# Kernel tuning notes

Measured on AMD Instinct MI355X. Metric: run time of the kernel, lower is better.

## Reference

```python
import jax, jax.numpy as jnp
import numpy as np

H, E, N, R = 1024, 2048, 16, 64  # hidden, expand, state, dt_rank
B, L = 2, 2048


def setup_inputs() -> dict:
    key = jax.random.key(0)
    ks = jax.random.split(key, 20)
    s = 0.02
    inp = {
        "x": jax.random.normal(ks[0], (B, L, H), jnp.float32),
        "ln_gamma": jnp.ones((H,), jnp.float32),
        "ln_beta": jnp.zeros((H,), jnp.float32),
        "W_in": jax.random.normal(ks[1], (H, 2 * E), jnp.float32) * s,
        "b_in": jnp.zeros((2 * E,), jnp.float32),
        "W_delta": jax.random.normal(ks[2], (E, R), jnp.float32) * s,
        "b_delta": jnp.zeros((R,), jnp.float32),
        "W_dt": jax.random.normal(ks[3], (R, E), jnp.float32) * s,
        "b_dt": jnp.zeros((E,), jnp.float32),
        "W_B": jax.random.normal(ks[4], (E, N), jnp.float32) * s,
        "b_B": jnp.zeros((N,), jnp.float32),
        "W_C": jax.random.normal(ks[5], (E, N), jnp.float32) * s,
        "b_C": jnp.zeros((N,), jnp.float32),
        "A_log": -jnp.exp(jax.random.normal(ks[6], (E, N), jnp.float32) * 0.1),
        "D": jax.random.normal(ks[7], (E,), jnp.float32) * 0.1,
        "W_out": jax.random.normal(ks[8], (E, H), jnp.float32) * s,
        "b_out": jnp.zeros((H,), jnp.float32),
    }
    return inp


def _layer_norm(x, gamma, beta, eps=1e-5):
    mu = jnp.mean(x, axis=-1, keepdims=True)
    var = jnp.var(x, axis=-1, keepdims=True)
    return (x - mu) * jax.lax.rsqrt(var + eps) * gamma + beta


def _selective_scan(x, delta, A, Bm, Cm):
    # x, delta: [B,L,E]; Bm, Cm: [B,L,N]; A: [E,N]
    def step(h, inputs):
        x_t, d_t, B_t, C_t = inputs  # [B,E],[B,E],[B,N],[B,N]
        A_disc = jnp.exp(d_t[..., None] * A)                     # [B,E,N]
        h = A_disc * h + d_t[..., None] * B_t[:, None, :] * x_t[..., None]
        y_t = jnp.einsum('bn,ben->be', C_t, h)
        return h, y_t

    h0 = jnp.zeros((x.shape[0], A.shape[0], A.shape[1]), x.dtype)
    xs = (jnp.swapaxes(x, 0, 1), jnp.swapaxes(delta, 0, 1),
          jnp.swapaxes(Bm, 0, 1), jnp.swapaxes(Cm, 0, 1))
    _, ys = jax.lax.scan(step, h0, xs)  # ys: [L,B,E]
    return jnp.swapaxes(ys, 0, 1)


def reference(x, ln_gamma, ln_beta, W_in, b_in, W_delta, b_delta, W_dt, b_dt,
              W_B, b_B, W_C, b_C, A_log, D, W_out, b_out):
    residual = x
    xn = _layer_norm(x, ln_gamma, ln_beta)
    x_proj = xn @ W_in + b_in                     # [B,L,2E]
    u, gate = jnp.split(x_proj, 2, axis=-1)
    u = jax.nn.silu(u)
    delta = jax.nn.softplus((u @ W_delta + b_delta) @ W_dt + b_dt)  # [B,L,E]
    Bm = u @ W_B + b_B                            # [B,L,N]
    Cm = u @ W_C + b_C                            # [B,L,N]
    A = -jnp.exp(A_log)                           # [E,N]
    y = _selective_scan(u, delta, A, Bm, Cm)
    y = y + u * D
    y = y * jax.nn.silu(gate)
    return y @ W_out + b_out + residual
```

## Files before the change

### kernel.cpp

```cpp
#include <hip/hip_runtime.h>
#include <stdint.h>

#define DH 1024
#define DE 2048
#define DN 16
#define DR 64
#define DB 2
#define DL 2048
#define DT (DB * DL)

typedef short short8 __attribute__((ext_vector_type(8)));
typedef float f32x4 __attribute__((ext_vector_type(4)));

__device__ __forceinline__ float bf2f(uint32_t u) {
  union { uint32_t i; float f; } v; v.i = u << 16; return v.f;
}
__device__ __forceinline__ unsigned short f2bf(float f) {
  union { float f; uint32_t i; } v; v.f = f;
  uint32_t r = v.i + 0x7FFFu + ((v.i >> 16) & 1u);
  return (unsigned short)(r >> 16);
}
__device__ __forceinline__ float ldsc(const void* p, size_t i, bool f32) {
  return f32 ? ((const float*)p)[i] : bf2f(((const unsigned short*)p)[i]);
}
__device__ __forceinline__ float4 ld4(const void* p, size_t i, bool f32) {
  if (f32) return *(const float4*)((const float*)p + i);
  ushort4 v = *(const ushort4*)((const unsigned short*)p + i);
  return make_float4(bf2f(v.x), bf2f(v.y), bf2f(v.z), bf2f(v.w));
}

__device__ __forceinline__ void gll16(const unsigned short* g, unsigned short* l) {
  __builtin_amdgcn_global_load_lds(
      (const __attribute__((address_space(1))) unsigned int*)g,
      (__attribute__((address_space(3))) unsigned int*)l, 16, 0, 0);
}

__device__ __forceinline__ void transpose_tile(
    const void* src, unsigned short* dst, int K, int N, int bx, int by,
    int tid, bool f32, float (*tile)[33]) {
  const int tx = tid & 31;
  const int ty = tid >> 5;
  const int kb = by * 32, nb = bx * 32;
  #pragma unroll
  for (int i = 0; i < 4; ++i)
    tile[ty + 8 * i][tx] = ldsc(src, (size_t)(kb + ty + 8 * i) * N + nb + tx, f32);
  __syncthreads();
  #pragma unroll
  for (int i = 0; i < 4; ++i)
    dst[(size_t)(nb + ty + 8 * i) * K + kb + tx] = f2bf(tile[tx][ty + 8 * i]);
}

__global__ __launch_bounds__(256) void k_convert_all(
    const void* __restrict__ W_in, const void* __restrict__ W_out,
    const void* __restrict__ W_dt, const void* __restrict__ Wd,
    const void* __restrict__ Wb, const void* __restrict__ Wc,
    const void* __restrict__ b_in, const void* __restrict__ b_out,
    const void* __restrict__ b_delta, const void* __restrict__ b_B,
    const void* __restrict__ b_C, const void* __restrict__ A_log,
    const void* __restrict__ Dvec, const void* __restrict__ b_dt,
    unsigned short* __restrict__ WtIn, unsigned short* __restrict__ WtOut,
    unsigned short* __restrict__ WtDt, unsigned short* __restrict__ WtDbc,
    float* __restrict__ bin, float* __restrict__ bout,
    float* __restrict__ bdbc, float* __restrict__ Ac, float* __restrict__ Dv,
    float* __restrict__ bdt,
    const uint32_t* __restrict__ probe) {
  const bool f32 = (probe[0] == 0x3F800000u);
  __shared__ float tile[32][33];
  const int tid = threadIdx.x;
  int f = blockIdx.x;
  if (f < 4096) {
    transpose_tile(W_in, WtIn, 1024, 4096, f & 127, f >> 7, tid, f32, tile);
    return;
  }
  f -= 4096;
  if (f < 2048) {
    transpose_tile(W_out, WtOut, 2048, 1024, f & 31, f >> 5, tid, f32, tile);
    return;
  }
  f -= 2048;
  if (f < 128) {
    transpose_tile(W_dt, WtDt, 64, 2048, f & 63, f >> 6, tid, f32, tile);
    return;
  }
  f -= 128;
  if (f < 1024) {
    const int idx = f * 256 + tid;
    const int c = idx >> 11, k = idx & 2047;
    float v = 0.f;
    if (c < 64) v = ldsc(Wd, (size_t)k * DR + c, f32);
    else if (c < 80) v = ldsc(Wb, (size_t)k * DN + (c - 64), f32);
    else if (c < 96) v = ldsc(Wc, (size_t)k * DN + (c - 80), f32);
    WtDbc[idx] = f2bf(v);
    return;
  }
  f -= 1024;
  {
    int i = f * 256 + tid;
    if (i < 4096) { bin[i] = ldsc(b_in, i, f32); return; }
    i -= 4096;
    if (i < 1024) { bout[i] = ldsc(b_out, i, f32); return; }
    i -= 1024;
    if (i < 128) {
      float v = 0.f;
      if (i < 64) v = ldsc(b_delta, i, f32);
      else if (i < 80) v = ldsc(b_B, i - 64, f32);
      else if (i < 96) v = ldsc(b_C, i - 80, f32);
      bdbc[i] = v; return;
    }
    i -= 128;
    if (i < 32768) { Ac[i] = -__expf(ldsc(A_log, i, f32)); return; }
    i -= 32768;
    if (i < 2048) { Dv[i] = ldsc(Dvec, i, f32); return; }
    i -= 2048;
    if (i < 2048) { bdt[i] = ldsc(b_dt, i, f32); }
  }
}

__global__ __launch_bounds__(256) void k_dbc_reduce(
    const float* __restrict__ Part, const float* __restrict__ bdbc,
    unsigned short* __restrict__ dt1b, float* __restrict__ dtBC, int MT) {
  const int gid = blockIdx.x * 256 + threadIdx.x;
  const int row = gid / 96, col = gid - row * 96;
  if (row >= MT) return;
  float s = bdbc[col];
  const size_t stride = (size_t)MT * 96;
  #pragma unroll
  for (int kp = 0; kp < 8; ++kp)
    s += Part[(size_t)kp * stride + (size_t)row * 96 + col];
  if (col < 64) dt1b[(size_t)row * 64 + col] = f2bf(s);
  else dtBC[(size_t)row * 32 + (col - 64)] = s;
}

__global__ __launch_bounds__(256) void k_delta(
    const unsigned short* __restrict__ A,
    const unsigned short* __restrict__ Wt,
    const float* __restrict__ bdt,
    unsigned short* __restrict__ Dout) {
  const int tid = threadIdx.x;
  const int wid = tid >> 6;
  const int lane = tid & 63;
  const int quad = lane >> 4;
  const int l16 = lane & 15;
  const int r0 = blockIdx.y * 32 + (wid & 1) * 16;
  const int c0 = blockIdx.x * 128 + (wid >> 1) * 64;

  const unsigned short* ap = A + (size_t)(r0 + l16) * 64 + quad * 8;
  const short8 a0 = *(const short8*)(ap);
  const short8 a1 = *(const short8*)(ap + 32);

  f32x4 acc[4];
  #pragma unroll
  for (int j = 0; j < 4; ++j) {
    acc[j][0] = 0.f; acc[j][1] = 0.f; acc[j][2] = 0.f; acc[j][3] = 0.f;
  }
  #pragma unroll
  for (int j = 0; j < 4; ++j) {
    const unsigned short* bp = Wt + (size_t)(c0 + j * 16 + l16) * 64 + quad * 8;
    const short8 b0 = *(const short8*)(bp);
    const short8 b1 = *(const short8*)(bp + 32);
    acc[j] = __builtin_amdgcn_mfma_f32_16x16x32_bf16(a0, b0, acc[j], 0, 0, 0);
    acc[j] = __builtin_amdgcn_mfma_f32_16x16x32_bf16(a1, b1, acc[j], 0, 0, 0);
  }
  #pragma unroll
  for (int j = 0; j < 4; ++j) {
    const int col = c0 + j * 16 + l16;
    const float bs = bdt[col];
    #pragma unroll
    for (int r = 0; r < 4; ++r) {
      const int row = r0 + quad * 4 + r;
      const float v = acc[j][r] + bs;
      const float sp = fmaxf(v, 0.f) + __logf(1.f + __expf(-fabsf(v)));
      Dout[(size_t)row * 2048 + col] = f2bf(sp);
    }
  }
}

__global__ __launch_bounds__(256) void k_out_reduce(
    const float* __restrict__ Part2, const float* __restrict__ bout,
    const void* __restrict__ resid, void* __restrict__ dout,
    int MT, int t0, int lgTc, const uint32_t* __restrict__ probe) {
  const bool f32 = (probe[0] == 0x3F800000u);
  const int gid = blockIdx.x * 256 + threadIdx.x;
  const int base = gid * 4;
  const int row = base >> 10;
  const int col = base & 1023;
  if (row >= MT) return;
  const int tcm = (1 << lgTc) - 1;
  const size_t grow = (size_t)((row >> lgTc) * DL + t0 + (row & tcm));
  const size_t ms = (size_t)MT * 1024;
  float4 p0 = *(const float4*)(Part2 + (size_t)row * 1024 + col);
  float4 p1 = *(const float4*)(Part2 + ms + (size_t)row * 1024 + col);
  float4 bo = *(const float4*)(bout + col);
  float4 rs = ld4(resid, grow * 1024 + col, f32);
  float4 o;
  o.x = p0.x + p1.x + bo.x + rs.x;
  o.y = p0.y + p1.y + bo.y + rs.y;
  o.z = p0.z + p1.z + bo.z + rs.z;
  o.w = p0.w + p1.w + bo.w + rs.w;
  if (f32) {
    *(float4*)((float*)dout + grow * 1024 + col) = o;
  } else {
    ushort4 u;
    u.x = f2bf(o.x); u.y = f2bf(o.y); u.z = f2bf(o.z); u.w = f2bf(o.w);
    *(ushort4*)((unsigned short*)dout + grow * 1024 + col) = u;
  }
}

__global__ __launch_bounds__(256) void ln_bf16(
    const void* __restrict__ x, const void* __restrict__ gamma,
    const void* __restrict__ beta, unsigned short* __restrict__ xn,
    int t0, int lgTc, const uint32_t* __restrict__ probe) {
  const bool f32 = (probe[0] == 0x3F800000u);
  const int row = blockIdx.x;
  const int tid = threadIdx.x;
  const int tcm = (1 << lgTc) - 1;
  const int grow = (row >> lgTc) * DL + t0 + (row & tcm);
  float4 v = ld4(x, (size_t)grow * DH + tid * 4, f32);
  float s = v.x + v.y + v.z + v.w;
  float ss = v.x * v.x + v.y * v.y + v.z * v.z + v.w * v.w;
  #pragma unroll
  for (int off = 32; off > 0; off >>= 1) {
    s += __shfl_down(s, off, 64);
    ss += __shfl_down(ss, off, 64);
  }
  __shared__ float sbuf[4], ssbuf[4];
  const int wave = tid >> 6, lane = tid & 63;
  if (lane == 0) { sbuf[wave] = s; ssbuf[wave] = ss; }
  __syncthreads();
  float tot = sbuf[0] + sbuf[1] + sbuf[2] + sbuf[3];
  float tots = ssbuf[0] + ssbuf[1] + ssbuf[2] + ssbuf[3];
  const float inv = 1.0f / (float)DH;
  float mu = tot * inv;
  float var = tots * inv - mu * mu;
  float rs = rsqrtf(var + 1e-5f);
  float4 gv = ld4(gamma, tid * 4, f32);
  float4 bv = ld4(beta, tid * 4, f32);
  ushort4 o;
  o.x = f2bf((v.x - mu) * rs * gv.x + bv.x);
  o.y = f2bf((v.y - mu) * rs * gv.y + bv.y);
  o.z = f2bf((v.z - mu) * rs * gv.z + bv.z);
  o.w = f2bf((v.w - mu) * rs * gv.w + bv.w);
  *(ushort4*)(xn + (size_t)row * DH + tid * 4) = o;
}

__global__ __launch_bounds__(256) void gemm_mfma(
    const unsigned short* __restrict__ A, int lda,
    const unsigned short* __restrict__ Wt,
    const float* __restrict__ bias,
    const void* __restrict__ resid,
    void* __restrict__ C, int ldc,
    int K, int mode, int t0, int lgTc,
    const uint32_t* __restrict__ probe) {
  __shared__ unsigned short As[2][4096];
  __shared__ unsigned short Bs[2][4096];
  const int tid = threadIdx.x;
  const int wid = tid >> 6;
  const int lane = tid & 63;
  const int quad = lane >> 4;
  const int l16 = lane & 15;
  const int wm = (wid & 1) * 64;
  const int wn = (wid >> 1) * 64;
  const int m0 = blockIdx.y * 128;
  int n0 = blockIdx.x * 128;
  int kbeg = 0, kend = K;
  if (mode == 5) {
    const int Ks = K >> 3; kbeg = blockIdx.x * Ks; kend = kbeg + Ks; n0 = 0;
  } else if (mode == 6) {
    const int Ks = K >> 1; const int kp = blockIdx.x >> 3;
    kbeg = kp * Ks; kend = kbeg + Ks; n0 = (blockIdx.x & 7) * 128;
  }
  const int sr = tid >> 2;
  const int sc = (tid & 3) * 8;

  const unsigned short* gA0 = A + (size_t)(m0 + sr) * lda + sc;
  const unsigned short* gA1 = A + (size_t)(m0 + sr + 64) * lda + sc;
  const unsigned short* gB0 = Wt + (size_t)(n0 + sr) * K + sc;
  const unsigned short* gB1 = Wt + (size_t)(n0 + sr + 64) * K + sc;
  const int wb = (tid & 192) * 8;
  unsigned short* lA00 = &As[0][wb];
  unsigned short* lA01 = &As[1][wb];
  unsigned short* lA10 = &As[0][2048 + wb];
  unsigned short* lA11 = &As[1][2048 + wb];
  unsigned short* lB00 = &Bs[0][wb];
  unsigned short* lB01 = &Bs[1][wb];
  unsigned short* lB10 = &Bs[0][2048 + wb];
  unsigned short* lB11 = &Bs[1][2048 + wb];

  f32x4 acc[4][4];
  #pragma unroll
  for (int i = 0; i < 4; ++i)
    #pragma unroll
    for (int j = 0; j < 4; ++j) {
      acc[i][j][0] = 0.f; acc[i][j][1] = 0.f;
      acc[i][j][2] = 0.f; acc[i][j][3] = 0.f;
    }

  for (int k0 = kbeg; k0 < kend; k0 += 64) {
    gll16(gA0 + k0, lA00);
    gll16(gA0 + k0 + 32, lA01);
    gll16(gA1 + k0, lA10);
    gll16(gA1 + k0 + 32, lA11);
    gll16(gB0 + k0, lB00);
    gll16(gB0 + k0 + 32, lB01);
    gll16(gB1 + k0, lB10);
    gll16(gB1 + k0 + 32, lB11);
    __syncthreads();
    #pragma unroll
    for (int ks = 0; ks < 2; ++ks) {
      short8 af[4], bf[4];
      #pragma unroll
      for (int i = 0; i < 4; ++i)
        af[i] = *(const short8*)(&As[ks][(wm + i * 16 + l16) * 32 + quad * 8]);
      #pragma unroll
      for (int j = 0; j < 4; ++j)
        bf[j] = *(const short8*)(&Bs[ks][(wn + j * 16 + l16) * 32 + quad * 8]);
      #pragma unroll
      for (int i = 0; i < 4; ++i)
        #pragma unroll
        for (int j = 0; j < 4; ++j)
          acc[i][j] = __builtin_amdgcn_mfma_f32_16x16x32_bf16(af[i], bf[j], acc[i][j], 0, 0, 0);
    }
    __syncthreads();
  }

  const int tcm = (1 << lgTc) - 1;
  const bool f32 = (probe[0] == 0x3F800000u);
  #pragma unroll
  for (int i = 0; i < 4; ++i) {
    #pragma unroll
    for (int j = 0; j < 4; ++j) {
      const int col = n0 + wn + j * 16 + l16;
      const float bsv = (mode == 5 || mode == 6) ? 0.f : bias[col];
      #pragma unroll
      for (int r = 0; r < 4; ++r) {
        const int row = m0 + wm + i * 16 + quad * 4 + r;
        float v = acc[i][j][r] + bsv;
        if (mode == 1) {
          if (col < DE) v = v / (1.f + __expf(-v));
          ((unsigned short*)C)[(size_t)row * ldc + col] = f2bf(v);
        } else if (mode == 2) {
          v = (v > 15.0f) ? v : log1pf(__expf(v));
          ((unsigned short*)C)[(size_t)row * ldc + col] = f2bf(v);
        } else if (mode == 5) {
          if (col < 96) {
            const size_t kpb = (size_t)blockIdx.x * ((size_t)gridDim.y * 128) * 96;
            ((float*)C)[kpb + (size_t)row * 96 + col] = v;
          }
        } else if (mode == 6) {
          const size_t kpb = (size_t)(blockIdx.x >> 3) * ((size_t)gridDim.y * 128) * 1024;
          ((float*)C)[kpb + (size_t)row * 1024 + col] = v;
        } else {
          const size_t grow = (size_t)((row >> lgTc) * DL + t0 + (row & tcm));
          v += ldsc(resid, grow * ldc + col, f32);
          if (f32) ((float*)C)[grow * ldc + col] = v;
          else ((unsigned short*)C)[grow * ldc + col] = f2bf(v);
        }
      }
    }
  }
}

__global__ __launch_bounds__(256) void scan_phaseA(
    const unsigned short* __restrict__ xproj,
    const unsigned short* __restrict__ delta,
    const float* __restrict__ dtBC,
    const float* __restrict__ Ac,
    float* __restrict__ Aprod,
    float* __restrict__ Hpart,
    int Tc, int P) {
  const int e = blockIdx.x * 256 + threadIdx.x;
  const int bs = blockIdx.y;
  const int S = Tc / P;
  const int b = bs / S, s = bs - b * S;
  const int r0 = b * Tc + s * P;

  float ac[16], ap[16], h[16];
  #pragma unroll
  for (int g = 0; g < 4; ++g) {
    const float4 a4 = *(const float4*)(Ac + (size_t)e * 16 + g * 4);
    ac[g * 4 + 0] = a4.x; ac[g * 4 + 1] = a4.y;
    ac[g * 4 + 2] = a4.z; ac[g * 4 + 3] = a4.w;
  }
  #pragma unroll
  for (int n = 0; n < 16; ++n) { ap[n] = 1.f; h[n] = 0.f; }

  const unsigned short* dp = delta + (size_t)r0 * 2048 + e;
  const unsigned short* xp = xproj + (size_t)r0 * 4096 + e;
  const float* bp = dtBC + (size_t)r0 * 32;

  for (int t = 0; t < P; ++t) {
    const float d = bf2f(*dp);
    const float x = bf2f(*xp);
    const float dx = d * x;
    #pragma unroll
    for (int g = 0; g < 4; ++g) {
      const float4 B = *(const float4*)(bp + g * 4);
      const float Bv[4] = {B.x, B.y, B.z, B.w};
      #pragma unroll
      for (int q = 0; q < 4; ++q) {
        const int n = g * 4 + q;
        const float a = __expf(d * ac[n]);
        ap[n] *= a;
        h[n] = a * h[n] + dx * Bv[q];
      }
    }
    dp += 2048; xp += 4096; bp += 32;
  }
  float* oA = Aprod + ((size_t)bs * 2048 + e) * 16;
  float* oH = Hpart + ((size_t)bs * 2048 + e) * 16;
  #pragma unroll
  for (int g = 0; g < 4; ++g) {
    *(float4*)(oA + g * 4) = make_float4(ap[g*4+0], ap[g*4+1], ap[g*4+2], ap[g*4+3]);
    *(float4*)(oH + g * 4) = make_float4(h[g*4+0], h[g*4+1], h[g*4+2], h[g*4+3]);
  }
}

__global__ __launch_bounds__(256) void scan_phaseB(
    const float* __restrict__ Aprod, const float* __restrict__ Hpart,
    float* __restrict__ Hstart,
    float* __restrict__ hstate,
    int S, int first) {
  const int gid = blockIdx.x * 256 + threadIdx.x;
  const int b = gid >> 13;
  const int en4 = gid & 8191;
  float4 h = first ? make_float4(0.f, 0.f, 0.f, 0.f)
                   : ((const float4*)hstate)[gid];
  for (int s = 0; s < S; ++s) {
    const size_t o = ((size_t)(b * S + s) << 13) + en4;
    ((float4*)Hstart)[o] = h;
    const float4 a = ((const float4*)Aprod)[o];
    const float4 p = ((const float4*)Hpart)[o];
    h.x = a.x * h.x + p.x;
    h.y = a.y * h.y + p.y;
    h.z = a.z * h.z + p.z;
    h.w = a.w * h.w + p.w;
  }
  ((float4*)hstate)[gid] = h;
}

__global__ __launch_bounds__(256) void scan_phaseC(
    unsigned short* __restrict__ xproj,
    const unsigned short* __restrict__ delta,
    const float* __restrict__ dtBC,
    const float* __restrict__ Ac,
    const float* __restrict__ Dv,
    const float* __restrict__ Hstart,
    int Tc, int P) {
  const int e = blockIdx.x * 256 + threadIdx.x;
  const int bs = blockIdx.y;
  const int S = Tc / P;
  const int b = bs / S, s = bs - b * S;
  const int r0 = b * Tc + s * P;

  float ac[16], h[16];
  #pragma unroll
  for (int g = 0; g < 4; ++g) {
    const float4 a4 = *(const float4*)(Ac + (size_t)e * 16 + g * 4);
    ac[g * 4 + 0] = a4.x; ac[g * 4 + 1] = a4.y;
    ac[g * 4 + 2] = a4.z; ac[g * 4 + 3] = a4.w;
    const float4 h4 = *(const float4*)(Hstart + ((size_t)bs * 2048 + e) * 16 + g * 4);
    h[g * 4 + 0] = h4.x; h[g * 4 + 1] = h4.y;
    h[g * 4 + 2] = h4.z; h[g * 4 + 3] = h4.w;
  }
  const float dv = Dv[e];

  const unsigned short* dp = delta + (size_t)r0 * 2048 + e;
  unsigned short* xp = xproj + (size_t)r0 * 4096 + e;
  const float* bp = dtBC + (size_t)r0 * 32;

  for (int t = 0; t < P; ++t) {
    const float d = bf2f(*dp);
    const float x = bf2f(xp[0]);
    const float dx = d * x;
    float y = 0.f;
    #pragma unroll
    for (int g = 0; g < 4; ++g) {
      const float4 B = *(const float4*)(bp + g * 4);
      const float4 Cc = *(const float4*)(bp + 16 + g * 4);
      const float Bv[4] = {B.x, B.y, B.z, B.w};
      const float Cv[4] = {Cc.x, Cc.y, Cc.z, Cc.w};
      #pragma unroll
      for (int q = 0; q < 4; ++q) {
        const int n = g * 4 + q;
        const float a = __expf(d * ac[n]);
        h[n] = a * h[n] + dx * Bv[q];
        y += Cv[q] * h[n];
      }
    }
    const float g = bf2f(xp[2048]);
    const float sg = g / (1.f + __expf(-g));
    xp[2048] = f2bf((y + x * dv) * sg);
    dp += 2048; xp += 4096; bp += 32;
  }
}

__global__ __launch_bounds__(256) void ln_kernel(
    const void* __restrict__ x, const void* __restrict__ gamma,
    const void* __restrict__ beta, float* __restrict__ xn,
    int t0, int lgTc, const uint32_t* __restrict__ probe) {
  const bool f32 = (probe[0] == 0x3F800000u);
  const int row = blockIdx.x;
  const int tid = threadIdx.x;
  const int tcm = (1 << lgTc) - 1;
  const int grow = (row >> lgTc) * DL + t0 + (row & tcm);
  float4 v = ld4(x, (size_t)grow * DH + tid * 4, f32);
  float s = v.x + v.y + v.z + v.w;
  float ss = v.x * v.x + v.y * v.y + v.z * v.z + v.w * v.w;
  #pragma unroll
  for (int off = 32; off > 0; off >>= 1) {
    s += __shfl_down(s, off, 64);
    ss += __shfl_down(ss, off, 64);
  }
  __shared__ float sbuf[4], ssbuf[4];
  const int wave = tid >> 6, lane = tid & 63;
  if (lane == 0) { sbuf[wave] = s; ssbuf[wave] = ss; }
  __syncthreads();
  float tot = sbuf[0] + sbuf[1] + sbuf[2] + sbuf[3];
  float tots = ssbuf[0] + ssbuf[1] + ssbuf[2] + ssbuf[3];
  const float inv = 1.0f / (float)DH;
  float mu = tot * inv;
  float var = tots * inv - mu * mu;
  float rs = rsqrtf(var + 1e-5f);
  float4 gv = ld4(gamma, tid * 4, f32);
  float4 bv = ld4(beta, tid * 4, f32);
  float4 o;
  o.x = (v.x - mu) * rs * gv.x + bv.x;
  o.y = (v.y - mu) * rs * gv.y + bv.y;
  o.z = (v.z - mu) * rs * gv.z + bv.z;
  o.w = (v.w - mu) * rs * gv.w + bv.w;
  *(float4*)(xn + (size_t)row * DH + tid * 4) = o;
}

#define BM 64
#define BN 64
#define BK 16
__global__ __launch_bounds__(256) void gemm_k(
    const float* __restrict__ A, int lda,
    const void* __restrict__ W,
    const void* __restrict__ bias,
    const void* __restrict__ resid,
    void* __restrict__ C, int ldc, int c_output,
    int N, int K, int mode, int t0, int lgTc,
    const uint32_t* __restrict__ probe) {
  const bool f32 = (probe[0] == 0x3F800000u);
  __shared__ float As[BM][BK + 1];
  __shared__ float Bs[BK][BN + 4];
  const int tid = threadIdx.x;
  const int tx = tid & 15;
  const int ty = tid >> 4;
  const int m0 = blockIdx.y * BM;
  const int n0 = blockIdx.x * BN;
  const int aRow = tid >> 2;
  const int aCol = (tid & 3) << 2;
  const int bRow = tid >> 4;
  const int bCol = (tid & 15) << 2;

  float acc[4][4];
  #pragma unroll
  for (int i = 0; i < 4; ++i)
    #pragma unroll
    for (int j = 0; j < 4; ++j) acc[i][j] = 0.f;

  for (int k0 = 0; k0 < K; k0 += BK) {
    float4 av = *(const float4*)(A + (size_t)(m0 + aRow) * lda + (k0 + aCol));
    As[aRow][aCol + 0] = av.x;
    As[aRow][aCol + 1] = av.y;
    As[aRow][aCol + 2] = av.z;
    As[aRow][aCol + 3] = av.w;
    if (n0 + bCol < N) {
      float4 bv = ld4(W, (size_t)(k0 + bRow) * N + (n0 + bCol), f32);
      Bs[bRow][bCol + 0] = bv.x;
      Bs[bRow][bCol + 1] = bv.y;
      Bs[bRow][bCol + 2] = bv.z;
      Bs[bRow][bCol + 3] = bv.w;
    } else {
      Bs[bRow][bCol + 0] = 0.f;
      Bs[bRow][bCol + 1] = 0.f;
      Bs[bRow][bCol + 2] = 0.f;
      Bs[bRow][bCol + 3] = 0.f;
    }
    __syncthreads();
    #pragma unroll
    for (int k = 0; k < BK; ++k) {
      float a0 = As[ty * 4 + 0][k];
      float a1 = As[ty * 4 + 1][k];
      float a2 = As[ty * 4 + 2][k];
      float a3 = As[ty * 4 + 3][k];
      float b0 = Bs[k][tx * 4 + 0];
      float b1 = Bs[k][tx * 4 + 1];
      float b2 = Bs[k][tx * 4 + 2];
      float b3 = Bs[k][tx * 4 + 3];
      acc[0][0] += a0 * b0; acc[0][1] += a0 * b1; acc[0][2] += a0 * b2; acc[0][3] += a0 * b3;
      acc[1][0] += a1 * b0; acc[1][1] += a1 * b1; acc[1][2] += a1 * b2; acc[1][3] += a1 * b3;
      acc[2][0] += a2 * b0; acc[2][1] += a2 * b1; acc[2][2] += a2 * b2; acc[2][3] += a2 * b3;
      acc[3][0] += a3 * b0; acc[3][1] += a3 * b1; acc[3][2] += a3 * b2; acc[3][3] += a3 * b3;
    }
    __syncthreads();
  }

  const int tcm = (1 << lgTc) - 1;
  #pragma unroll
  for (int i = 0; i < 4; ++i) {
    const int gm = m0 + ty * 4 + i;
    #pragma unroll
    for (int j = 0; j < 4; ++j) {
      const int gn = n0 + tx * 4 + j;
      if (gn < N) {
        float v = acc[i][j] + ldsc(bias, gn, f32);
        size_t crow = (size_t)gm;
        if (mode == 1) {
          if (gn < DE) v = v / (1.0f + __expf(-v));
        } else if (mode == 2) {
          v = (v > 15.0f) ? v : log1pf(__expf(v));
        } else if (mode == 3) {
          const size_t grow = (size_t)((gm >> lgTc) * DL + t0 + (gm & tcm));
          v += ldsc(resid, grow * ldc + gn, f32);
          crow = grow;
        }
        if (c_output) {
          if (f32) ((float*)C)[crow * ldc + gn] = v;
          else ((unsigned short*)C)[crow * ldc + gn] = f2bf(v);
        } else {
          ((float*)C)[crow * ldc + gn] = v;
        }
      }
    }
  }
}

__global__ __launch_bounds__(256) void scan_kernel(
    float* __restrict__ xproj, const float* __restrict__ delta,
    const float* __restrict__ Bmat, const float* __restrict__ Cmat,
    const void* __restrict__ A_log, const void* __restrict__ Dvec,
    float* __restrict__ hstate, int Tc, int first,
    const uint32_t* __restrict__ probe) {
  const bool f32 = (probe[0] == 0x3F800000u);
  const int gid = blockIdx.x * 256 + threadIdx.x;
  const int b = gid >> 11;
  const int e = gid & (DE - 1);
  float Ac[DN];
  #pragma unroll
  for (int n = 0; n < DN; ++n) Ac[n] = -__expf(ldsc(A_log, (size_t)e * DN + n, f32));
  const float Dvl = ldsc(Dvec, e, f32);
  float h[DN];
  float* hs = hstate + ((size_t)b * DE + e) * DN;
  if (first) {
    #pragma unroll
    for (int n = 0; n < DN; ++n) h[n] = 0.f;
  } else {
    #pragma unroll
    for (int n = 0; n < DN; ++n) h[n] = hs[n];
  }
  for (int t = 0; t < Tc; ++t) {
    const size_t r = (size_t)(b * Tc + t);
    const float x = xproj[r * (2 * DE) + e];
    const float g = xproj[r * (2 * DE) + DE + e];
    const float d = delta[r * DE + e];
    const float4* bp = (const float4*)(Bmat + r * DN);
    const float4* cp = (const float4*)(Cmat + r * DN);
    float4 b0 = bp[0], b1 = bp[1], b2 = bp[2], b3 = bp[3];
    float4 c0 = cp[0], c1 = cp[1], c2 = cp[2], c3 = cp[3];
    float Bv[DN] = {b0.x,b0.y,b0.z,b0.w, b1.x,b1.y,b1.z,b1.w,
                    b2.x,b2.y,b2.z,b2.w, b3.x,b3.y,b3.z,b3.w};
    float Cv[DN] = {c0.x,c0.y,c0.z,c0.w, c1.x,c1.y,c1.z,c1.w,
                    c2.x,c2.y,c2.z,c2.w, c3.x,c3.y,c3.z,c3.w};
    const float dx = d * x;
    float y = 0.f;
    #pragma unroll
    for (int n = 0; n < DN; ++n) {
      float ad = __expf(d * Ac[n]);
      h[n] = ad * h[n] + dx * Bv[n];
      y += Cv[n] * h[n];
    }
    const float sg = g / (1.0f + __expf(-g));
    xproj[r * (2 * DE) + DE + e] = (y + x * Dvl) * sg;
  }
  #pragma unroll
  for (int n = 0; n < DN; ++n) hs[n] = h[n];
}

extern "C" void kernel_launch(void* const* d_in, const int* in_sizes, int n_in,
                              void* d_out, int out_size, void* d_ws, size_t ws_size,
                              hipStream_t stream) {
  const void* x = d_in[0];
  const void* ln_gamma = d_in[1];
  const void* ln_beta = d_in[2];
  const void* W_in = d_in[3];
  const void* b_in = d_in[4];
  const void* W_delta = d_in[5];
  const void* b_delta = d_in[6];
  const void* W_dt = d_in[7];
  const void* b_dt = d_in[8];
  const void* W_B = d_in[9];
  const void* b_B = d_in[10];
  const void* W_C = d_in[11];
  const void* b_C = d_in[12];
  const void* A_log = d_in[13];
  const void* Dvec = d_in[14];
  const void* W_out = d_in[15];
  const void* b_out = d_in[16];
  const uint32_t* probe = (const uint32_t*)ln_gamma;
  char* ws = (char*)d_ws;

  const size_t P_WTIN = (size_t)4096 * 1024 * 2;
  const size_t P_WTOUT = (size_t)1024 * 2048 * 2;
  const size_t P_WDBC = (size_t)128 * 2048 * 2;
  const size_t P_WDT = (size_t)2048 * 64 * 2;
  const size_t P_F32 = (size_t)(4096 + 1024 + 128 + 32768 + 2048 + 2048 + 65536) * 4;
  const size_t persist = P_WTIN + P_WTOUT + P_WDBC + P_WDT + P_F32;
  auto chunk_bytes = [](int Tc) {
    const int P = Tc < 64 ? Tc : 64;
    const size_t S = (size_t)(Tc / P);
    const size_t MT = (size_t)DB * Tc;
    size_t tail = MT * (2048 * 2 + 8 * 96 * 4) + 3 * (size_t)DB * S * 32768 * 4;
    size_t part2 = MT * 8192;
    if (part2 > tail) tail = part2;
    return MT * ((1024 + 4096 + 64) * 2 + 32 * 4) + tail;
  };
  int lgTc = -1;
  for (int lg = 11; lg >= 6; --lg) {
    if (persist + chunk_bytes(1 << lg) + 4096 <= ws_size) { lgTc = lg; break; }
  }

  if (lgTc >= 0) {
    const int Tc = 1 << lgTc;
    const int MT = DB * Tc;
    const int nchunks = DL / Tc;
    const int P = Tc < 64 ? Tc : 64;
    const int S = Tc / P;

    size_t off = 0;
    unsigned short* WtIn = (unsigned short*)(ws + off); off += P_WTIN;
    unsigned short* WtOut = (unsigned short*)(ws + off); off += P_WTOUT;
    unsigned short* WtDbc = (unsigned short*)(ws + off); off += P_WDBC;
    unsigned short* WtDt = (unsigned short*)(ws + off); off += P_WDT;
    float* bin = (float*)(ws + off); off += 4096 * 4;
    float* bout = (float*)(ws + off); off += 1024 * 4;
    float* bdbc = (float*)(ws + off); off += 128 * 4;
    float* bdt = (float*)(ws + off); off += 2048 * 4;
    float* Ac = (float*)(ws + off); off += 32768 * 4;
    float* Dv = (float*)(ws + off); off += 2048 * 4;
    float* hstate = (float*)(ws + off); off += 65536 * 4;
    unsigned short* xn = (unsigned short*)(ws + off); off += (size_t)MT * 1024 * 2;
    unsigned short* xproj = (unsigned short*)(ws + off); off += (size_t)MT * 4096 * 2;
    unsigned short* dt1b = (unsigned short*)(ws + off); off += (size_t)MT * 64 * 2;
    float* dtBC = (float*)(ws + off); off += (size_t)MT * 32 * 4;
    char* alias0 = ws + off;
    unsigned short* delta = (unsigned short*)(alias0);
    float* Part = (float*)(alias0 + (size_t)MT * 2048 * 2);
    float* Aprod = (float*)(alias0 + (size_t)MT * 2048 * 2 + (size_t)8 * MT * 96 * 4);
    float* Hpart = Aprod + (size_t)DB * S * 32768;
    float* Hstart = Hpart + (size_t)DB * S * 32768;
    float* Part2 = (float*)(alias0);

    k_convert_all<<<7469, 256, 0, stream>>>(
        W_in, W_out, W_dt, W_delta, W_B, W_C,
        b_in, b_out, b_delta, b_B, b_C, A_log, Dvec, b_dt,
        WtIn, WtOut, WtDt, WtDbc, bin, bout, bdbc, Ac, Dv, bdt, probe);

    for (int c = 0; c < nchunks; ++c) {
      const int t0 = c * Tc;
      ln_bf16<<<MT, 256, 0, stream>>>(x, ln_gamma, ln_beta, xn, t0, lgTc, probe);
      gemm_mfma<<<dim3(4096 / 128, MT / 128), 256, 0, stream>>>(
          xn, 1024, WtIn, bin, nullptr, xproj, 4096, 1024, 1, 0, 0, probe);
      gemm_mfma<<<dim3(8, MT / 128), 256, 0, stream>>>(
          xproj, 4096, WtDbc, bdbc, nullptr, Part, 96, 2048, 5, 0, 0, probe);
      k_dbc_reduce<<<(MT * 96 + 255) / 256, 256, 0, stream>>>(
          Part, bdbc, dt1b, dtBC, MT);
      k_delta<<<dim3(2048 / 128, MT / 32), 256, 0, stream>>>(
          dt1b, WtDt, bdt, delta);
      scan_phaseA<<<dim3(2048 / 256, DB * S), 256, 0, stream>>>(
          xproj, delta, dtBC, Ac, Aprod, Hpart, Tc, P);
      scan_phaseB<<<64, 256, 0, stream>>>(
          Aprod, Hpart, Hstart, hstate, S, c == 0 ? 1 : 0);
      scan_phaseC<<<dim3(2048 / 256, DB * S), 256, 0, stream>>>(
          xproj, delta, dtBC, Ac, Dv, Hstart, Tc, P);
      gemm_mfma<<<dim3(16, MT / 128), 256, 0, stream>>>(
          xproj + DE, 4096, WtOut, bout, nullptr, Part2, 1024, 2048, 6, 0, 0, probe);
      k_out_reduce<<<MT, 256, 0, stream>>>(
          Part2, bout, x, d_out, MT, t0, lgTc, probe);
    }
    return;
  }

  {
    int lg = 8;
    while (lg > 6 &&
           ((size_t)(2u << lg) * 7264 * 4 + (size_t)DB * DE * DN * 4 + 4096) > ws_size)
      --lg;
    const int Tc = 1 << lg;
    const int MT = DB * Tc;
    const int nchunks = DL / Tc;

    size_t off = 0;
    float* xproj_c = (float*)(ws + off); off += (size_t)MT * 2 * DE * 4;
    float* xn_c    = (float*)(ws + off); off += (size_t)MT * DH * 4;
    float* delta_c = (float*)(ws + off); off += (size_t)MT * DE * 4;
    float* dt1_c   = (float*)(ws + off); off += (size_t)MT * DR * 4;
    float* Bm_c    = (float*)(ws + off); off += (size_t)MT * DN * 4;
    float* Cm_c    = (float*)(ws + off); off += (size_t)MT * DN * 4;
    float* hstate  = (float*)(ws + off);

    for (int c = 0; c < nchunks; ++c) {
      const int t0 = c * Tc;
      ln_kernel<<<MT, 256, 0, stream>>>(x, ln_gamma, ln_beta, xn_c, t0, lg, probe);
      gemm_k<<<dim3(2 * DE / BN, MT / BM), 256, 0, stream>>>(
          xn_c, DH, W_in, b_in, nullptr, xproj_c, 2 * DE, 0, 2 * DE, DH, 1, 0, 0, probe);
      gemm_k<<<dim3(1, MT / BM), 256, 0, stream>>>(
          xproj_c, 2 * DE, W_delta, b_delta, nullptr, dt1_c, DR, 0, DR, DE, 0, 0, 0, probe);
      gemm_k<<<dim3(DE / BN, MT / BM), 256, 0, stream>>>(
          dt1_c, DR, W_dt, b_dt, nullptr, delta_c, DE, 0, DE, DR, 2, 0, 0, probe);
      gemm_k<<<dim3(1, MT / BM), 256, 0, stream>>>(
          xproj_c, 2 * DE, W_B, b_B, nullptr, Bm_c, DN, 0, DN, DE, 0, 0, 0, probe);
      gemm_k<<<dim3(1, MT / BM), 256, 0, stream>>>(
          xproj_c, 2 * DE, W_C, b_C, nullptr, Cm_c, DN, 0, DN, DE, 0, 0, 0, probe);
      scan_kernel<<<16, 256, 0, stream>>>(
          xproj_c, delta_c, Bm_c, Cm_c, A_log, Dvec, hstate, Tc, c == 0 ? 1 : 0, probe);
      gemm_k<<<dim3(DH / BN, MT / BM), 256, 0, stream>>>(
          xproj_c + DE, 2 * DE, W_out, b_out, x, d_out, DH, 1, DH, DE, 3, t0, lg, probe);
    }
  }
}
```

Measured before the change: 409.0 us.

## Add dedicated 256x256-tile MFMA kernel for input projection GEMM

Adds a specialized 512-thread kernel that computes the input projection with 256x256 output tiles and 64-wide K steps, using direct global-to-LDS loads and bf16 MFMA, with SiLU fused for the u half. It replaces the generic 128x128 gemm_mfma when the token count is a multiple of 256. Larger tiles raise arithmetic intensity and reduce redundant global loads, but they use more registers and LDS, and produce fewer blocks, which can hurt occupancy. The loop loads into LDS and synchronizes without double buffering, so load latency is not overlapped with compute.

```diff
diff --git a/kernel.cpp b/kernel.cpp
--- a/kernel.cpp
+++ b/kernel.cpp
@@ -360,6 +360,95 @@
   }
 }
 
+__global__ __launch_bounds__(512) void k_inproj256(
+    const unsigned short* __restrict__ A,
+    const unsigned short* __restrict__ Wt,
+    const float* __restrict__ bias,
+    unsigned short* __restrict__ C) {
+  __shared__ unsigned short As[2][8192];
+  __shared__ unsigned short Bs[2][8192];
+  const int tid = threadIdx.x;
+  const int wid = tid >> 6;
+  const int lane = tid & 63;
+  const int quad = lane >> 4;
+  const int l16 = lane & 15;
+  const int wr = (wid >> 2) * 128;
+  const int wc = (wid & 3) * 64;
+  const int m0 = blockIdx.y * 256;
+  const int n0 = blockIdx.x * 256;
+  const int K = 1024;
+
+  const int sr = tid >> 2;
+  const int sc = (tid & 3) * 8;
+  const unsigned short* gA0 = A + (size_t)(m0 + sr) * K + sc;
+  const unsigned short* gA1 = A + (size_t)(m0 + 128 + sr) * K + sc;
+  const unsigned short* gB0 = Wt + (size_t)(n0 + sr) * K + sc;
+  const unsigned short* gB1 = Wt + (size_t)(n0 + 128 + sr) * K + sc;
+  const int wb = wid * 512;
+  unsigned short* lA00 = &As[0][wb];
+  unsigned short* lA01 = &As[1][wb];
+  unsigned short* lA10 = &As[0][4096 + wb];
+  unsigned short* lA11 = &As[1][4096 + wb];
+  unsigned short* lB00 = &Bs[0][wb];
+  unsigned short* lB01 = &Bs[1][wb];
+  unsigned short* lB10 = &Bs[0][4096 + wb];
+  unsigned short* lB11 = &Bs[1][4096 + wb];
+
+  f32x4 acc[8][4];
+  #pragma unroll
+  for (int i = 0; i < 8; ++i)
+    #pragma unroll
+    for (int j = 0; j < 4; ++j) {
+      acc[i][j][0] = 0.f; acc[i][j][1] = 0.f;
+      acc[i][j][2] = 0.f; acc[i][j][3] = 0.f;
+    }
+
+  for (int k0 = 0; k0 < K; k0 += 64) {
+    gll16(gA0 + k0, lA00);
+    gll16(gA0 + k0 + 32, lA01);
+    gll16(gA1 + k0, lA10);
+    gll16(gA1 + k0 + 32, lA11);
+    gll16(gB0 + k0, lB00);
+    gll16(gB0 + k0 + 32, lB01);
+    gll16(gB1 + k0, lB10);
+    gll16(gB1 + k0 + 32, lB11);
+    __syncthreads();
+    #pragma unroll
+    for (int ks = 0; ks < 2; ++ks) {
+      short8 af[8], bf[4];
+      #pragma unroll
+      for (int i = 0; i < 8; ++i)
+        af[i] = *(const short8*)(&As[ks][(wr + i * 16 + l16) * 32 + quad * 8]);
+      #pragma unroll
+      for (int j = 0; j < 4; ++j)
+        bf[j] = *(const short8*)(&Bs[ks][(wc + j * 16 + l16) * 32 + quad * 8]);
+      #pragma unroll
+      for (int i = 0; i < 8; ++i)
+        #pragma unroll
+        for (int j = 0; j < 4; ++j)
+          acc[i][j] = __builtin_amdgcn_mfma_f32_16x16x32_bf16(af[i], bf[j], acc[i][j], 0, 0, 0);
+    }
+    __syncthreads();
+  }
+
+  #pragma unroll
+  for (int j = 0; j < 4; ++j) {
+    const int col = n0 + wc + j * 16 + l16;
+    const float bsv = bias[col];
+    const bool dos = (col < DE);
+    #pragma unroll
+    for (int i = 0; i < 8; ++i) {
+      #pragma unroll
+      for (int r = 0; r < 4; ++r) {
+        const int row = m0 + wr + i * 16 + quad * 4 + r;
+        float v = acc[i][j][r] + bsv;
+        if (dos) v = v / (1.f + __expf(-v));
+        C[(size_t)row * 4096 + col] = f2bf(v);
+      }
+    }
+  }
+}
+
 __global__ __launch_bounds__(256) void scan_phaseA(
     const unsigned short* __restrict__ xproj,
     const unsigned short* __restrict__ delta,
@@ -761,8 +850,13 @@
     for (int c = 0; c < nchunks; ++c) {
       const int t0 = c * Tc;
       ln_bf16<<<MT, 256, 0, stream>>>(x, ln_gamma, ln_beta, xn, t0, lgTc, probe);
-      gemm_mfma<<<dim3(4096 / 128, MT / 128), 256, 0, stream>>>(
-          xn, 1024, WtIn, bin, nullptr, xproj, 4096, 1024, 1, 0, 0, probe);
+      if ((MT & 255) == 0) {
+        k_inproj256<<<dim3(4096 / 256, MT / 256), 512, 0, stream>>>(
+            xn, WtIn, bin, xproj);
+      } else {
+        gemm_mfma<<<dim3(4096 / 128, MT / 128), 256, 0, stream>>>(
+            xn, 1024, WtIn, bin, nullptr, xproj, 4096, 1024, 1, 0, 0, probe);
+      }
       gemm_mfma<<<dim3(8, MT / 128), 256, 0, stream>>>(
           xproj, 4096, WtDbc, bdbc, nullptr, Part, 96, 2048, 5, 0, 0, probe);
       k_dbc_reduce<<<(MT * 96 + 255) / 256, 256, 0, stream>>>(
```

Result: faster. 394.9 us (-3.4%).
